# Kernel optimization log

Measured on AMD Instinct MI355X. Metric: run time of the kernel, lower is better.

The kernel has to match this reference:

```python
import jax, jax.numpy as jnp
import numpy as np

VOCAB = 50000
EMB = 100
HID = 128
NPROD = 10000
PEMB = 50
B, T = 256, 512
IN = EMB + PEMB  # 150


def setup_inputs() -> dict:
    key = jax.random.key(0)
    ks = jax.random.split(key, 10)
    s = 1.0 / np.sqrt(HID)  # torch LSTM init scale
    emb = jax.random.normal(ks[0], (VOCAB, EMB), jnp.float32)
    emb = emb.at[0].set(0.0)  # padding_idx=0
    return {
        "review": jax.random.randint(ks[1], (B, T), 0, VOCAB),
        "product": jax.random.randint(ks[2], (B,), 0, NPROD),
        "embedding": emb,
        "product_embedding": jax.random.normal(ks[3], (NPROD, PEMB), jnp.float32),
        "W_ih": jax.random.uniform(ks[4], (4 * HID, IN), jnp.float32, -s, s),
        "W_hh": jax.random.uniform(ks[5], (4 * HID, HID), jnp.float32, -s, s),
        "b_ih": jax.random.uniform(ks[6], (4 * HID,), jnp.float32, -s, s),
        "b_hh": jax.random.uniform(ks[7], (4 * HID,), jnp.float32, -s, s),
        "fc_w": jax.random.uniform(ks[8], (1, HID), jnp.float32, -s, s),
        "fc_b": jax.random.uniform(ks[9], (1,), jnp.float32, -s, s),
    }


def _lstm_last_h(x_proj, W_hh):
    # x_proj: [T, B, 4H] = precomputed input projection + biases
    def step(carry, xg):
        h, c = carry
        gates = xg + h @ W_hh.T  # [B, 4H]
        i, f, g, o = jnp.split(gates, 4, axis=-1)  # torch gate order i,f,g,o
        i, f, o = jax.nn.sigmoid(i), jax.nn.sigmoid(f), jax.nn.sigmoid(o)
        g = jnp.tanh(g)
        c = f * c + i * g
        h = o * jnp.tanh(c)
        return (h, c), None

    b = x_proj.shape[1]
    init = (jnp.zeros((b, HID), x_proj.dtype), jnp.zeros((b, HID), x_proj.dtype))
    (h, _), _ = jax.lax.scan(step, init, x_proj)
    return h  # [B, H] — hidden state at last timestep


def reference(review, product, embedding, product_embedding, W_ih, W_hh, b_ih, b_hh, fc_w, fc_b):
    er = embedding[review]                       # [B, T, EMB]
    ep = product_embedding[product][:, None, :]  # [B, 1, PEMB]
    ep = jnp.broadcast_to(ep, (er.shape[0], er.shape[1], PEMB))
    combined = jnp.concatenate([er, ep], axis=-1)  # [B, T, IN]
    # precompute input projection for all timesteps in one GEMM
    x_proj = jnp.einsum('btd,gd->tbg', combined, W_ih) + (b_ih + b_hh)  # [T, B, 4H]
    h_last = _lstm_last_h(x_proj, W_hh)
    out = h_last @ fc_w.T + fc_b  # [B, 1]
    return jax.nn.sigmoid(out)
```

## Files before the change

### kernel.cpp

```cpp
#include <hip/hip_runtime.h>
#include <hip/hip_bf16.h>
#include <math.h>

#define VOCAB 50000
#define EMB 100
#define HID 128
#define NPROD 10000
#define PEMB 50
#define BSZ 256
#define TLEN 512
#define INDIM 150
#define G4 512

typedef __attribute__((ext_vector_type(4))) float f32x4;

__device__ __forceinline__ float sigm(float x) {
    return __builtin_amdgcn_rcpf(1.f + __expf(-x));
}
__device__ __forceinline__ float tanh_fast(float x) {
    float e = __expf(-2.f * fabsf(x));
    float r = (1.f - e) * __builtin_amdgcn_rcpf(1.f + e);
    return __builtin_copysignf(r, x);
}

__global__ void k_transpose(const float* __restrict__ W_ih, float* __restrict__ Wt) {
    int idx = blockIdx.x * blockDim.x + threadIdx.x;
    if (idx < INDIM * G4) {
        int d = idx / G4, g = idx % G4;
        Wt[idx] = W_ih[g * INDIM + d];
    }
}

__global__ void k_pbias(const int* __restrict__ product,
                        const float* __restrict__ pemb,
                        const float* __restrict__ Wt,
                        const float* __restrict__ b_ih,
                        const float* __restrict__ b_hh,
                        float* __restrict__ pbias) {
    __shared__ float ep_s[PEMB];
    int b = blockIdx.x;
    int tid = threadIdx.x;
    int p = product[b];
    if (tid < PEMB) ep_s[tid] = pemb[p * PEMB + tid];
    __syncthreads();
    int g0 = tid, g1 = tid + 256;
    float a0 = b_ih[g0] + b_hh[g0];
    float a1 = b_ih[g1] + b_hh[g1];
    #pragma unroll 5
    for (int d = 0; d < PEMB; ++d) {
        float e = ep_s[d];
        a0 += e * Wt[(EMB + d) * G4 + g0];
        a1 += e * Wt[(EMB + d) * G4 + g1];
    }
    pbias[b * G4 + g0] = a0;
    pbias[b * G4 + g1] = a1;
}

__global__ void k_table(const float* __restrict__ emb,
                        const float* __restrict__ Wt,
                        float* __restrict__ table) {
    __shared__ __align__(16) float es[16 * EMB];
    int v0 = blockIdx.x * 16;
    int tid = threadIdx.x;
    for (int l = tid; l < 16 * EMB; l += 256) es[l] = emb[v0 * EMB + l];
    __syncthreads();
    float acc0[16], acc1[16];
    #pragma unroll
    for (int r = 0; r < 16; ++r) { acc0[r] = 0.f; acc1[r] = 0.f; }
    #pragma unroll 5
    for (int k4 = 0; k4 < EMB / 4; ++k4) {
        float w0[4], w1[4];
        #pragma unroll
        for (int j = 0; j < 4; ++j) {
            w0[j] = Wt[(k4 * 4 + j) * G4 + tid];
            w1[j] = Wt[(k4 * 4 + j) * G4 + tid + 256];
        }
        #pragma unroll
        for (int r = 0; r < 16; ++r) {
            float4 e = *reinterpret_cast<const float4*>(&es[r * EMB + k4 * 4]);
            acc0[r] += e.x * w0[0] + e.y * w0[1] + e.z * w0[2] + e.w * w0[3];
            acc1[r] += e.x * w1[0] + e.y * w1[1] + e.z * w1[2] + e.w * w1[3];
        }
    }
    #pragma unroll
    for (int r = 0; r < 16; ++r) {
        table[(v0 + r) * G4 + tid]       = acc0[r];
        table[(v0 + r) * G4 + tid + 256] = acc1[r];
    }
}

__global__ __launch_bounds__(512, 2) void k_lstm(
    const int* __restrict__ review,
    const float* __restrict__ W_hh,
    const float* __restrict__ table,
    const float* __restrict__ pbias,
    const float* __restrict__ fc_w,
    const float* __restrict__ fc_b,
    float* __restrict__ out) {
    __shared__ __align__(16) float hsA[HID];
    __shared__ __align__(16) float hsB[HID];
    __shared__ float gsh[G4];
    __shared__ int rv_s[TLEN];
    int b = blockIdx.x;
    int g = threadIdx.x;
    int wgate = g >> 7;
    int u = g & 127;

    rv_s[g] = review[b * TLEN + g];
    if (g < HID) { hsA[g] = 0.f; hsB[g] = 0.f; }
    __syncthreads();

    float x_cur = table[rv_s[0] * G4 + g];
    float pb = pbias[b * G4 + g];

    float w[128];
    #pragma unroll
    for (int j = 0; j < 32; ++j) {
        f32x4 t = *reinterpret_cast<const f32x4*>(W_hh + g * HID + 4 * j);
        w[4 * j + 0] = t.x; w[4 * j + 1] = t.y; w[4 * j + 2] = t.z; w[4 * j + 3] = t.w;
    }
    #pragma unroll
    for (int k = 0; k < 128; ++k) asm volatile("" : "+v"(w[k]));

    const float* hr = hsA;
    float* hw = hsB;
    float c = 0.f;

    for (int t = 0; t < TLEN; ++t) {
        float x_next = table[rv_s[(t + 1) & (TLEN - 1)] * G4 + g];

        float a0 = 0.f, a1 = 0.f, a2 = 0.f, a3 = 0.f;
        #pragma unroll
        for (int j = 0; j < 32; ++j) {
            f32x4 h4 = *reinterpret_cast<const f32x4*>(&hr[4 * j]);
            a0 += h4.x * w[4 * j + 0];
            a1 += h4.y * w[4 * j + 1];
            a2 += h4.z * w[4 * j + 2];
            a3 += h4.w * w[4 * j + 3];
        }
        float pre = x_cur + pb + ((a0 + a1) + (a2 + a3));
        float act = (wgate == 2) ? tanh_fast(pre) : sigm(pre);
        gsh[g] = act;
        __syncthreads();

        float gi = gsh[u];
        float gf = gsh[HID + u];
        float gg = gsh[2 * HID + u];
        float go = gsh[3 * HID + u];
        c = gf * c + gi * gg;
        float h = go * tanh_fast(c);
        if (g < HID) hw[g] = h;
        __syncthreads();

        const float* tmp = hr; hr = hw; hw = (float*)tmp;
        x_cur = x_next;
    }

    if (g < 64) {
        float v = hr[g] * fc_w[g] + hr[g + 64] * fc_w[g + 64];
        #pragma unroll
        for (int off = 32; off >= 1; off >>= 1) v += __shfl_xor(v, off);
        if (g == 0) out[b] = sigm(v + fc_b[0]);
    }
}

extern "C" void kernel_launch(void* const* d_in, const int* in_sizes, int n_in,
                              void* d_out, int out_size, void* d_ws, size_t ws_size,
                              hipStream_t stream) {
    const int*   review  = (const int*)d_in[0];
    const int*   product = (const int*)d_in[1];
    const float* emb     = (const float*)d_in[2];
    const float* pemb    = (const float*)d_in[3];
    const float* W_ih    = (const float*)d_in[4];
    const float* W_hh    = (const float*)d_in[5];
    const float* b_ih    = (const float*)d_in[6];
    const float* b_hh    = (const float*)d_in[7];
    const float* fc_w    = (const float*)d_in[8];
    const float* fc_b    = (const float*)d_in[9];
    float* out = (float*)d_out;

    char* ws = (char*)d_ws;
    float* Wt    = (float*)(ws);
    float* pbias = (float*)(ws + 307200);
    float* table = (float*)(ws + 831488);

    k_transpose<<<(INDIM * G4 + 255) / 256, 256, 0, stream>>>(W_ih, Wt);
    k_pbias<<<BSZ, 256, 0, stream>>>(product, pemb, Wt, b_ih, b_hh, pbias);
    k_table<<<VOCAB / 16, 256, 0, stream>>>(emb, Wt, table);
    k_lstm<<<BSZ, 512, 0, stream>>>(review, W_hh, table, pbias, fc_w, fc_b, out);
}
```

Before: 653.3 us.

## Split each LSTM gate dot product across two threads with 1024-thread blocks

The recurrent kernel now uses two threads per gate row. Each thread holds half of the W_hh row in registers and computes half of the h·W dot product, and the two halves are combined with a lane shuffle. This halves the per-thread serial FMA chain and the register footprint on the latency-bound sequential loop. In exchange, each block is twice as large, with more threads taking part in every barrier, and a shuffle is added to each timestep.

```diff
diff --git a/kernel.cpp b/kernel.cpp
--- a/kernel.cpp
+++ b/kernel.cpp
@@ -89,7 +89,7 @@
     }
 }
 
-__global__ __launch_bounds__(512, 2) void k_lstm(
+__global__ __launch_bounds__(1024, 4) void k_lstm(
     const int* __restrict__ review,
     const float* __restrict__ W_hh,
     const float* __restrict__ table,
@@ -102,25 +102,25 @@
     __shared__ float gsh[G4];
     __shared__ int rv_s[TLEN];
     int b = blockIdx.x;
-    int g = threadIdx.x;
+    int t0 = threadIdx.x;
+    int g = t0 >> 1;
+    int half = t0 & 1;
     int wgate = g >> 7;
-    int u = g & 127;
 
-    rv_s[g] = review[b * TLEN + g];
-    if (g < HID) { hsA[g] = 0.f; hsB[g] = 0.f; }
+    if (t0 < TLEN) rv_s[t0] = review[b * TLEN + t0];
+    if (t0 < HID) { hsA[t0] = 0.f; hsB[t0] = 0.f; }
     __syncthreads();
 
     float x_cur = table[rv_s[0] * G4 + g];
     float pb = pbias[b * G4 + g];
 
-    float w[128];
+    f32x4 w4[16];
+    const float* wrow = W_hh + g * HID + half * 64;
     #pragma unroll
-    for (int j = 0; j < 32; ++j) {
-        f32x4 t = *reinterpret_cast<const f32x4*>(W_hh + g * HID + 4 * j);
-        w[4 * j + 0] = t.x; w[4 * j + 1] = t.y; w[4 * j + 2] = t.z; w[4 * j + 3] = t.w;
-    }
+    for (int j = 0; j < 16; ++j)
+        w4[j] = *reinterpret_cast<const f32x4*>(wrow + 4 * j);
     #pragma unroll
-    for (int k = 0; k < 128; ++k) asm volatile("" : "+v"(w[k]));
+    for (int j = 0; j < 16; ++j) asm volatile("" : "+v"(w4[j]));
 
     const float* hr = hsA;
     float* hw = hsB;
@@ -130,37 +130,41 @@
         float x_next = table[rv_s[(t + 1) & (TLEN - 1)] * G4 + g];
 
         float a0 = 0.f, a1 = 0.f, a2 = 0.f, a3 = 0.f;
+        const float* hb = hr + half * 64;
         #pragma unroll
-        for (int j = 0; j < 32; ++j) {
-            f32x4 h4 = *reinterpret_cast<const f32x4*>(&hr[4 * j]);
-            a0 += h4.x * w[4 * j + 0];
-            a1 += h4.y * w[4 * j + 1];
-            a2 += h4.z * w[4 * j + 2];
-            a3 += h4.w * w[4 * j + 3];
+        for (int j = 0; j < 16; ++j) {
+            f32x4 h4 = *reinterpret_cast<const f32x4*>(hb + 4 * j);
+            a0 += h4.x * w4[j].x;
+            a1 += h4.y * w4[j].y;
+            a2 += h4.z * w4[j].z;
+            a3 += h4.w * w4[j].w;
         }
-        float pre = x_cur + pb + ((a0 + a1) + (a2 + a3));
+        float a = (a0 + a1) + (a2 + a3);
+        a += __shfl_xor(a, 1);
+        float pre = x_cur + pb + a;
         float act = (wgate == 2) ? tanh_fast(pre) : sigm(pre);
         gsh[g] = act;
         __syncthreads();
 
-        float gi = gsh[u];
-        float gf = gsh[HID + u];
-        float gg = gsh[2 * HID + u];
-        float go = gsh[3 * HID + u];
-        c = gf * c + gi * gg;
-        float h = go * tanh_fast(c);
-        if (g < HID) hw[g] = h;
+        if (t0 < HID) {
+            float gi = gsh[t0];
+            float gf = gsh[HID + t0];
+            float gg = gsh[2 * HID + t0];
+            float go = gsh[3 * HID + t0];
+            c = gf * c + gi * gg;
+            hw[t0] = go * tanh_fast(c);
+        }
         __syncthreads();
 
         const float* tmp = hr; hr = hw; hw = (float*)tmp;
         x_cur = x_next;
     }
 
-    if (g < 64) {
-        float v = hr[g] * fc_w[g] + hr[g + 64] * fc_w[g + 64];
+    if (t0 < 64) {
+        float v = hr[t0] * fc_w[t0] + hr[t0 + 64] * fc_w[t0 + 64];
         #pragma unroll
         for (int off = 32; off >= 1; off >>= 1) v += __shfl_xor(v, off);
-        if (g == 0) out[b] = sigm(v + fc_b[0]);
+        if (t0 == 0) out[b] = sigm(v + fc_b[0]);
     }
 }
 
@@ -187,5 +191,5 @@
     k_transpose<<<(INDIM * G4 + 255) / 256, 256, 0, stream>>>(W_ih, Wt);
     k_pbias<<<BSZ, 256, 0, stream>>>(product, pemb, Wt, b_ih, b_hh, pbias);
     k_table<<<VOCAB / 16, 256, 0, stream>>>(emb, Wt, table);
-    k_lstm<<<BSZ, 512, 0, stream>>>(review, W_hh, table, pbias, fc_w, fc_b, out);
+    k_lstm<<<BSZ, 1024, 0, stream>>>(review, W_hh, table, pbias, fc_w, fc_b, out);
 }
```

After: 837.5 us. 1.28x slower.
